# Performance work log

Measured on AMD Instinct MI355X. Metric: run time of the kernel, lower is better.

The kernel has to match this reference:

```python
import jax, jax.numpy as jnp
import numpy as np

BIG = 1e9  # finite stand-in for float('inf') border padding (grad-safe)


def setup_inputs() -> dict:
    key = jax.random.key(0)
    k1, k2 = jax.random.split(key)
    B, L1, L2, F = 32, 1024, 1024, 128
    return {
        "seq1": jax.random.normal(k1, (B, L1, F), dtype=jnp.float32),
        "seq2": jax.random.normal(k2, (B, L2, F), dtype=jnp.float32),
        "scale_weights": jnp.ones((1,), dtype=jnp.float32),  # nn.Parameter ones(num_scales)/num_scales -> softmax-normalized anyway
    }


def _dtw_similarity(seq1, seq2):
    """Vectorized (anti-diagonal wavefront) version of MultiScaleDTW._compute_dtw.

    Same recurrence: D[i,j] = ||s1[i-1]-s2[j-1]|| + min(D[i-1,j-1], D[i-1,j], D[i,j-1]),
    D[0,0]=0, first row/col = inf. Returns similarity = 1/(1 + D[L1,L2]/(L1+L2)).
    """
    B, L1, F = seq1.shape
    L2 = seq2.shape[1]
    # pairwise L2 distance matrix (B, L1, L2) via |a|^2 + |b|^2 - 2 a.b (one GEMM)
    sq1 = jnp.sum(seq1 * seq1, axis=-1)
    sq2 = jnp.sum(seq2 * seq2, axis=-1)
    dot = jnp.einsum('bif,bjf->bij', seq1, seq2)
    C = jnp.sqrt(jnp.maximum(sq1[:, :, None] + sq2[:, None, :] - 2.0 * dot, 0.0))

    i_idx = jnp.arange(L1 + 1)
    # diagonal k holds D[i, k-i] for i in [0, L1]
    d0 = jnp.full((B, L1 + 1), BIG, jnp.float32).at[:, 0].set(0.0)  # k=0: D[0,0]=0
    d1 = jnp.full((B, L1 + 1), BIG, jnp.float32)                     # k=1: borders = inf

    def shift(x):  # x[:, i] -> x[:, i-1], pad with BIG
        return jnp.concatenate([jnp.full((B, 1), BIG, x.dtype), x[:, :-1]], axis=1)

    def step(carry, k):
        prev2, prev = carry  # diagonals k-2, k-1
        j = k - i_idx
        row = jnp.clip(i_idx - 1, 0, L1 - 1)
        col = jnp.clip(j - 1, 0, L2 - 1)
        c = C[:, row, col]  # (B, L1+1) cost along the diagonal
        m = jnp.minimum(shift(prev2), jnp.minimum(shift(prev), prev))
        cur = c + m
        valid = (i_idx >= 1) & (i_idx <= L1) & (j >= 1) & (j <= L2)
        cur = jnp.where(valid[None, :], cur, BIG)
        return (prev, cur), None

    (_, last), _ = jax.lax.scan(step, (d0, d1), jnp.arange(2, L1 + L2 + 1))
    dtw_dist = last[:, L1] / (L1 + L2)  # D[L1, L2] / (L1 + L2)
    return 1.0 / (1.0 + dtw_dist)


def reference(seq1, seq2, scale_weights):
    # num_scales = 1: softmax over single scale weight -> 1.0; only scale-0 DTW runs
    w = jax.nn.softmax(scale_weights, axis=0)
    sim = _dtw_similarity(seq1, seq2)
    return w[0] * sim  # combined_similarity, shape (B,)
```

## Files before the change

### kernel.cpp

```cpp
#include <hip/hip_runtime.h>
#include <hip/hip_bf16.h>

#define BIGV 1.0e9f

static constexpr int B_ = 32;
static constexpr int L_ = 1024;
static constexpr int F_ = 128;
static constexpr int S_ = 4;
static constexpr int SKEW_U = 1296;
static constexpr size_t SKEW_PB = (size_t)SKEW_U * 1024;
static constexpr size_t OFF_N1 = (size_t)B_ * SKEW_PB;
static constexpr size_t OFF_N2 = OFF_N1 + (size_t)B_ * L_;
static constexpr int NSEG_ = 80;

typedef __attribute__((ext_vector_type(8))) short short8;
typedef __attribute__((ext_vector_type(4))) float f32x4;

__device__ __forceinline__ unsigned pack2(float x, float y) {
  union { float f; unsigned u; } a, b;
  a.f = x; b.f = y;
  unsigned lo = (a.u + 0x7FFFu + ((a.u >> 16) & 1u)) >> 16;
  unsigned hi = (b.u + 0x7FFFu + ((b.u >> 16) & 1u)) >> 16;
  return lo | (hi << 16);
}

__global__ void norm_kernel(const float* __restrict__ s1, const float* __restrict__ s2,
                            float* __restrict__ ws) {
  int gt   = blockIdx.x * blockDim.x + threadIdx.x;
  int wid  = gt >> 6;
  int lane = gt & 63;
  const float* src = (wid < B_ * L_) ? (s1 + (size_t)wid * F_)
                                     : (s2 + (size_t)(wid - B_ * L_) * F_);
  float2 v = ((const float2*)src)[lane];
  float s = v.x * v.x + v.y * v.y;
#pragma unroll
  for (int o = 32; o > 0; o >>= 1) s += __shfl_xor(s, o, 64);
  if (lane == 0) ws[OFF_N1 + wid] = s;
}

__global__ __launch_bounds__(256) void cost_kernel(const float* __restrict__ s1,
                                                   const float* __restrict__ s2,
                                                   float* __restrict__ ws) {
  __shared__ short aL[128][136];
  __shared__ short bL[128][136];
  __shared__ float q1[128], q2[128];

  const int tid = threadIdx.x;
  const int b   = blockIdx.y;
  const int tc  = blockIdx.x & 7;
  const int tr  = blockIdx.x >> 3;

  const float* Ap = s1 + (size_t)b * L_ * F_ + (size_t)tr * 128 * F_;
  const float* Bp = s2 + (size_t)b * L_ * F_ + (size_t)tc * 128 * F_;

#pragma unroll 4
  for (int it = 0; it < 16; ++it) {
    int idx = it * 1024 + tid * 4;
    int r = idx >> 7, cc = idx & 127;
    float4 va = *(const float4*)(Ap + idx);
    float4 vb = *(const float4*)(Bp + idx);
    *(uint2*)&aL[r][cc] = make_uint2(pack2(va.x, va.y), pack2(va.z, va.w));
    *(uint2*)&bL[r][cc] = make_uint2(pack2(vb.x, vb.y), pack2(vb.z, vb.w));
  }
  if (tid < 128) q1[tid] = ws[OFF_N1 + (size_t)b * L_ + tr * 128 + tid];
  else           q2[tid - 128] = ws[OFF_N2 + (size_t)b * L_ + tc * 128 + (tid - 128)];
  __syncthreads();

  const int wave = tid >> 6, lane = tid & 63, quad = lane >> 4, l16 = lane & 15;
  const int m0 = (wave >> 1) * 64, n0 = (wave & 1) * 64;

  f32x4 acc[4][4] = {};
#pragma unroll
  for (int kc = 0; kc < 4; ++kc) {
    short8 af[4], bf[4];
#pragma unroll
    for (int mi = 0; mi < 4; ++mi)
      af[mi] = *(const short8*)&aL[m0 + mi * 16 + l16][kc * 32 + quad * 8];
#pragma unroll
    for (int nj = 0; nj < 4; ++nj)
      bf[nj] = *(const short8*)&bL[n0 + nj * 16 + l16][kc * 32 + quad * 8];
#pragma unroll
    for (int mi = 0; mi < 4; ++mi)
#pragma unroll
      for (int nj = 0; nj < 4; ++nj)
        acc[mi][nj] = __builtin_amdgcn_mfma_f32_16x16x32_bf16(af[mi], bf[nj], acc[mi][nj], 0, 0, 0);
  }

  float* Cb = ws + (size_t)b * SKEW_PB;
#pragma unroll
  for (int mi = 0; mi < 4; ++mi)
#pragma unroll
    for (int nj = 0; nj < 4; ++nj) {
      int lr0 = m0 + mi * 16 + quad * 4;
      int lc  = n0 + nj * 16 + l16;
      int r0  = tr * 128 + lr0;
      int c   = tc * 128 + lc;
      float4 v;
      v.x = sqrtf(fmaxf(q1[lr0 + 0] + q2[lc] - 2.0f * acc[mi][nj][0], 0.0f));
      v.y = sqrtf(fmaxf(q1[lr0 + 1] + q2[lc] - 2.0f * acc[mi][nj][1], 0.0f));
      v.z = sqrtf(fmaxf(q1[lr0 + 2] + q2[lc] - 2.0f * acc[mi][nj][2], 0.0f));
      v.w = sqrtf(fmaxf(q1[lr0 + 3] + q2[lc] - 2.0f * acc[mi][nj][3], 0.0f));
      *(float4*)&Cb[(size_t)(c + S_ * (r0 >> 4)) * 1024 + r0] = v;
    }
}

__global__ __launch_bounds__(320, 1) void dtw_kernel(const float* __restrict__ ws,
                                                     float* __restrict__ out) {
  __shared__ float colLds[32][1024];

  const int b    = blockIdx.x;
  const int tid  = threadIdx.x;
  const int wave = tid >> 6;
  const int lane = tid & 63;
  const float* Cb = ws + (size_t)b * SKEW_PB;

  if (wave != 0) {
    const int rbase = (wave - 1) * 4;
    auto loadSeg = [&](int g) {
#pragma unroll
      for (int i = 0; i < 4; ++i) {
        int u = g * 16 + rbase + i;
        const float4* src = (const float4*)(Cb + (size_t)u * 1024);
        float4* dst = (float4*)&colLds[u & 31][0];
#pragma unroll
        for (int q = 0; q < 4; ++q) dst[q * 64 + lane] = src[q * 64 + lane];
      }
    };
    loadSeg(0);
    for (int s = 0; s < NSEG_; ++s) {
      __syncthreads();
      if (s < NSEG_ - 1) loadSeg(s + 1);
    }
    return;
  }

  float left[16];
#pragma unroll
  for (int r = 0; r < 16; ++r) left[r] = BIGV;
  float bot = BIGV;
  float sh[4] = {BIGV, BIGV, BIGV, BIGV};
  float result = 0.0f;
  const bool l0 = (lane == 0);
  int col = -S_ * lane;
  float4 pre[2][4];

  for (int s = 0; s < NSEG_; ++s) {
    __syncthreads();
    {
      const float4* rp0 = (const float4*)&colLds[(16 * s) & 31][lane * 16];
      const float4* rp1 = (const float4*)&colLds[(16 * s + 1) & 31][lane * 16];
#pragma unroll
      for (int q = 0; q < 4; ++q) { pre[0][q] = rp0[q]; pre[1][q] = rp1[q]; }
    }
#pragma unroll
    for (int k = 0; k < 16; ++k) {
      const int t = 16 * s + k;
      float shN = __shfl_up(bot, 1, 64);

      const float4* cb = pre[k & 1];
      float cv[16] = { cb[0].x, cb[0].y, cb[0].z, cb[0].w,
                       cb[1].x, cb[1].y, cb[1].z, cb[1].w,
                       cb[2].x, cb[2].y, cb[2].z, cb[2].w,
                       cb[3].x, cb[3].y, cb[3].z, cb[3].w };

      if (k < 14) {
        const float4* rp = (const float4*)&colLds[(t + 2) & 31][lane * 16];
#pragma unroll
        for (int q = 0; q < 4; ++q) pre[k & 1][q] = rp[q];
      }

      float dgT = l0 ? ((t == 0) ? 0.0f : BIGV) : sh[k & 3];
      float upT = l0 ? BIGV : sh[(k + 1) & 3];
      bool act = ((unsigned)col < 1024u);
      float c0 = act ? cv[0] : BIGV;
      float cur = c0 + fminf(fminf(dgT, upT), left[0]);
      float nl[16];
      nl[0] = cur;
#pragma unroll
      for (int r = 1; r < 16; ++r) {
        cur = cv[r] + fminf(fminf(left[r - 1], left[r]), cur);
        nl[r] = cur;
      }
#pragma unroll
      for (int r = 0; r < 16; ++r) left[r] = nl[r];
      bot = nl[15];
      sh[k & 3] = shN;

      if (t == 1275) result = bot;
      col += 1;
    }
  }
  if (lane == 63) out[b] = 1.0f / (1.0f + result * (1.0f / 2048.0f));
}

extern "C" void kernel_launch(void* const* d_in, const int* in_sizes, int n_in,
                              void* d_out, int out_size, void* d_ws, size_t ws_size,
                              hipStream_t stream) {
  const float* s1 = (const float*)d_in[0];
  const float* s2 = (const float*)d_in[1];
  float* out = (float*)d_out;
  float* ws  = (float*)d_ws;

  norm_kernel<<<dim3((2 * B_ * L_) / 4), 256, 0, stream>>>(s1, s2, ws);
  cost_kernel<<<dim3(64, B_), 256, 0, stream>>>(s1, s2, ws);
  dtw_kernel<<<dim3(B_), 320, 0, stream>>>(ws, out);
}
```

Measured before the change: 262.8 us.

## Split DTW wavefront across two lagged waves and store cost matrix as bf16

```diff
diff --git a/kernel.cpp b/kernel.cpp
--- a/kernel.cpp
+++ b/kernel.cpp
@@ -7,11 +7,11 @@
 static constexpr int L_ = 1024;
 static constexpr int F_ = 128;
 static constexpr int S_ = 4;
-static constexpr int SKEW_U = 1296;
-static constexpr size_t SKEW_PB = (size_t)SKEW_U * 1024;
-static constexpr size_t OFF_N1 = (size_t)B_ * SKEW_PB;
-static constexpr size_t OFF_N2 = OFF_N1 + (size_t)B_ * L_;
-static constexpr int NSEG_ = 80;
+static constexpr int UDIM_ = 1280;
+static constexpr int LAG_ = 288;
+static constexpr int NSEGL_ = 80;
+static constexpr int NSEGG_ = 98;
+static constexpr size_t STREAM_US = (size_t)B_ * 2 * UDIM_ * 512;
 
 typedef __attribute__((ext_vector_type(8))) short short8;
 typedef __attribute__((ext_vector_type(4))) float f32x4;
@@ -25,7 +25,7 @@
 }
 
 __global__ void norm_kernel(const float* __restrict__ s1, const float* __restrict__ s2,
-                            float* __restrict__ ws) {
+                            float* __restrict__ nrm) {
   int gt   = blockIdx.x * blockDim.x + threadIdx.x;
   int wid  = gt >> 6;
   int lane = gt & 63;
@@ -35,12 +35,13 @@
   float s = v.x * v.x + v.y * v.y;
 #pragma unroll
   for (int o = 32; o > 0; o >>= 1) s += __shfl_xor(s, o, 64);
-  if (lane == 0) ws[OFF_N1 + wid] = s;
+  if (lane == 0) nrm[wid] = s;
 }
 
 __global__ __launch_bounds__(256) void cost_kernel(const float* __restrict__ s1,
                                                    const float* __restrict__ s2,
-                                                   float* __restrict__ ws) {
+                                                   ushort* __restrict__ stream,
+                                                   const float* __restrict__ nrm) {
   __shared__ short aL[128][136];
   __shared__ short bL[128][136];
   __shared__ float q1[128], q2[128];
@@ -62,8 +63,8 @@
     *(uint2*)&aL[r][cc] = make_uint2(pack2(va.x, va.y), pack2(va.z, va.w));
     *(uint2*)&bL[r][cc] = make_uint2(pack2(vb.x, vb.y), pack2(vb.z, vb.w));
   }
-  if (tid < 128) q1[tid] = ws[OFF_N1 + (size_t)b * L_ + tr * 128 + tid];
-  else           q2[tid - 128] = ws[OFF_N2 + (size_t)b * L_ + tc * 128 + (tid - 128)];
+  if (tid < 128) q1[tid] = nrm[(size_t)b * L_ + tr * 128 + tid];
+  else           q2[tid - 128] = nrm[(size_t)B_ * L_ + (size_t)b * L_ + tc * 128 + (tid - 128)];
   __syncthreads();
 
   const int wave = tid >> 6, lane = tid & 63, quad = lane >> 4, l16 = lane & 15;
@@ -86,7 +87,7 @@
         acc[mi][nj] = __builtin_amdgcn_mfma_f32_16x16x32_bf16(af[mi], bf[nj], acc[mi][nj], 0, 0, 0);
   }
 
-  float* Cb = ws + (size_t)b * SKEW_PB;
+  ushort* Sb = stream + (size_t)(b * 2) * UDIM_ * 512;
 #pragma unroll
   for (int mi = 0; mi < 4; ++mi)
 #pragma unroll
@@ -95,113 +96,133 @@
       int lc  = n0 + nj * 16 + l16;
       int r0  = tr * 128 + lr0;
       int c   = tc * 128 + lc;
-      float4 v;
-      v.x = sqrtf(fmaxf(q1[lr0 + 0] + q2[lc] - 2.0f * acc[mi][nj][0], 0.0f));
-      v.y = sqrtf(fmaxf(q1[lr0 + 1] + q2[lc] - 2.0f * acc[mi][nj][1], 0.0f));
-      v.z = sqrtf(fmaxf(q1[lr0 + 2] + q2[lc] - 2.0f * acc[mi][nj][2], 0.0f));
-      v.w = sqrtf(fmaxf(q1[lr0 + 3] + q2[lc] - 2.0f * acc[mi][nj][3], 0.0f));
-      *(float4*)&Cb[(size_t)(c + S_ * (r0 >> 4)) * 1024 + r0] = v;
+      float vx = sqrtf(fmaxf(q1[lr0 + 0] + q2[lc] - 2.0f * acc[mi][nj][0], 0.0f));
+      float vy = sqrtf(fmaxf(q1[lr0 + 1] + q2[lc] - 2.0f * acc[mi][nj][1], 0.0f));
+      float vz = sqrtf(fmaxf(q1[lr0 + 2] + q2[lc] - 2.0f * acc[mi][nj][2], 0.0f));
+      float vw = sqrtf(fmaxf(q1[lr0 + 3] + q2[lc] - 2.0f * acc[mi][nj][3], 0.0f));
+      int w  = r0 >> 9;
+      int rl = r0 & 511;
+      int u  = c + 4 * (rl >> 3);
+      ushort* p = Sb + ((size_t)w * UDIM_ + u) * 512 + rl;
+      *(uint2*)p = make_uint2(pack2(vx, vy), pack2(vz, vw));
     }
 }
 
-__global__ __launch_bounds__(320, 1) void dtw_kernel(const float* __restrict__ ws,
+__global__ __launch_bounds__(256, 1) void dtw_kernel(const ushort* __restrict__ stream,
                                                      float* __restrict__ out) {
-  __shared__ float colLds[32][1024];
+  __shared__ ushort ldsA[2][16][512];
+  __shared__ ushort ldsB[2][16][512];
+  __shared__ float hand[1024];
 
   const int b    = blockIdx.x;
   const int tid  = threadIdx.x;
   const int wave = tid >> 6;
   const int lane = tid & 63;
-  const float* Cb = ws + (size_t)b * SKEW_PB;
-
-  if (wave != 0) {
-    const int rbase = (wave - 1) * 4;
-    auto loadSeg = [&](int g) {
-#pragma unroll
-      for (int i = 0; i < 4; ++i) {
-        int u = g * 16 + rbase + i;
-        const float4* src = (const float4*)(Cb + (size_t)u * 1024);
-        float4* dst = (float4*)&colLds[u & 31][0];
-#pragma unroll
-        for (int q = 0; q < 4; ++q) dst[q * 64 + lane] = src[q * 64 + lane];
+
+  if (wave >= 2) {
+    const int ls = wave - 2;
+    const ushort* src = stream + (size_t)(b * 2 + ls) * UDIM_ * 512;
+    auto loadSeg = [&](int g, int buf) {
+      ushort(*dst)[512] = ls ? ldsB[buf] : ldsA[buf];
+#pragma unroll
+      for (int i = 0; i < 16; ++i) {
+        const uint4* sp = (const uint4*)(src + (size_t)(g * 16 + i) * 512);
+        *(uint4*)&dst[i][lane * 8] = sp[lane];
       }
     };
-    loadSeg(0);
-    for (int s = 0; s < NSEG_; ++s) {
+    if (ls == 0) loadSeg(0, 0);
+    for (int n = 0; n < NSEGG_; ++n) {
       __syncthreads();
-      if (s < NSEG_ - 1) loadSeg(s + 1);
+      int g = (ls == 0) ? (n + 1) : (n - 17);
+      if ((unsigned)g < (unsigned)NSEGL_) loadSeg(g, g & 1);
     }
     return;
   }
 
-  float left[16];
-#pragma unroll
-  for (int r = 0; r < 16; ++r) left[r] = BIGV;
+  const int w = wave;
+  const bool l0 = (lane == 0);
+
+  float left[8];
+#pragma unroll
+  for (int r = 0; r < 8; ++r) left[r] = BIGV;
   float bot = BIGV;
   float sh[4] = {BIGV, BIGV, BIGV, BIGV};
-  float result = 0.0f;
-  const bool l0 = (lane == 0);
-  int col = -S_ * lane;
-  float4 pre[2][4];
-
-  for (int s = 0; s < NSEG_; ++s) {
+  float hPrev = BIGV, result = 0.0f;
+  uint4 pre[2];
+
+  for (int n = 0; n < NSEGG_; ++n) {
     __syncthreads();
-    {
-      const float4* rp0 = (const float4*)&colLds[(16 * s) & 31][lane * 16];
-      const float4* rp1 = (const float4*)&colLds[(16 * s + 1) & 31][lane * 16];
-#pragma unroll
-      for (int q = 0; q < 4; ++q) { pre[0][q] = rp0[q]; pre[1][q] = rp1[q]; }
-    }
+    const int sBase = 16 * n - (w ? LAG_ : 0);
+    if ((unsigned)sBase >= 1280u) continue;
+
+    const int buf = (sBase >> 4) & 1;
+    const ushort(*lds)[512] = w ? ldsB[buf] : ldsA[buf];
+    pre[0] = *(const uint4*)&lds[0][lane * 8];
+    pre[1] = *(const uint4*)&lds[1][lane * 8];
+
 #pragma unroll
     for (int k = 0; k < 16; ++k) {
-      const int t = 16 * s + k;
+      const int s = sBase + k;
+      const int col = s - S_ * lane;
       float shN = __shfl_up(bot, 1, 64);
-
-      const float4* cb = pre[k & 1];
-      float cv[16] = { cb[0].x, cb[0].y, cb[0].z, cb[0].w,
-                       cb[1].x, cb[1].y, cb[1].z, cb[1].w,
-                       cb[2].x, cb[2].y, cb[2].z, cb[2].w,
-                       cb[3].x, cb[3].y, cb[3].z, cb[3].w };
-
-      if (k < 14) {
-        const float4* rp = (const float4*)&colLds[(t + 2) & 31][lane * 16];
-#pragma unroll
-        for (int q = 0; q < 4; ++q) pre[k & 1][q] = rp[q];
-      }
-
-      float dgT = l0 ? ((t == 0) ? 0.0f : BIGV) : sh[k & 3];
-      float upT = l0 ? BIGV : sh[(k + 1) & 3];
+      float hCur = hand[s & 1023];
+
+      uint4 cw = pre[k & 1];
+      if (k < 14) pre[k & 1] = *(const uint4*)&lds[k + 2][lane * 8];
+
+      float cv[8];
+      cv[0] = __uint_as_float(cw.x << 16);
+      cv[1] = __uint_as_float(cw.x & 0xFFFF0000u);
+      cv[2] = __uint_as_float(cw.y << 16);
+      cv[3] = __uint_as_float(cw.y & 0xFFFF0000u);
+      cv[4] = __uint_as_float(cw.z << 16);
+      cv[5] = __uint_as_float(cw.z & 0xFFFF0000u);
+      cv[6] = __uint_as_float(cw.w << 16);
+      cv[7] = __uint_as_float(cw.w & 0xFFFF0000u);
+
+      float dgT = sh[k & 3];
+      float upT = sh[(k + 1) & 3];
+      if (l0) {
+        if (w == 0) { dgT = (s == 0) ? 0.0f : BIGV; upT = BIGV; }
+        else        { dgT = (s == 0) ? BIGV : hPrev; upT = hCur; }
+      }
       bool act = ((unsigned)col < 1024u);
       float c0 = act ? cv[0] : BIGV;
       float cur = c0 + fminf(fminf(dgT, upT), left[0]);
-      float nl[16];
+      float nl[8];
       nl[0] = cur;
 #pragma unroll
-      for (int r = 1; r < 16; ++r) {
+      for (int r = 1; r < 8; ++r) {
         cur = cv[r] + fminf(fminf(left[r - 1], left[r]), cur);
         nl[r] = cur;
       }
 #pragma unroll
-      for (int r = 0; r < 16; ++r) left[r] = nl[r];
-      bot = nl[15];
+      for (int r = 0; r < 8; ++r) left[r] = nl[r];
+      bot = nl[7];
       sh[k & 3] = shN;
-
-      if (t == 1275) result = bot;
-      col += 1;
+      hPrev = hCur;
+
+      if (w == 0) {
+        int j = s - 252;
+        if (lane == 63 && (unsigned)j < 1024u) hand[j] = bot;
+      } else if (s == 1275) {
+        result = bot;
+      }
     }
   }
-  if (lane == 63) out[b] = 1.0f / (1.0f + result * (1.0f / 2048.0f));
+  if (w == 1 && lane == 63) out[b] = 1.0f / (1.0f + result * (1.0f / 2048.0f));
 }
 
 extern "C" void kernel_launch(void* const* d_in, const int* in_sizes, int n_in,
                               void* d_out, int out_size, void* d_ws, size_t ws_size,
-                              hipStream_t stream) {
+                              hipStream_t stream_) {
   const float* s1 = (const float*)d_in[0];
   const float* s2 = (const float*)d_in[1];
   float* out = (float*)d_out;
-  float* ws  = (float*)d_ws;
-
-  norm_kernel<<<dim3((2 * B_ * L_) / 4), 256, 0, stream>>>(s1, s2, ws);
-  cost_kernel<<<dim3(64, B_), 256, 0, stream>>>(s1, s2, ws);
-  dtw_kernel<<<dim3(B_), 320, 0, stream>>>(ws, out);
-}
+  ushort* cws = (ushort*)d_ws;
+  float* nrm = (float*)(cws + STREAM_US);
+
+  norm_kernel<<<dim3((2 * B_ * L_) / 4), 256, 0, stream_>>>(s1, s2, nrm);
+  cost_kernel<<<dim3(64, B_), 256, 0, stream_>>>(s1, s2, cws, nrm);
+  dtw_kernel<<<dim3(B_), 256, 0, stream_>>>(cws, out);
+}
```

Measured after the change: 320.5 us. +21.9%, slower.
